# Optimization experiments

Hardware: AMD Instinct MI355X
Metric: run time of the kernel (lower is better)

The kernel has to match this reference:

```python
import jax, jax.numpy as jnp
import numpy as np

QLEN, BSZ, D_MODEL = 2048, 4, 1024
N_HEAD, D_HEAD = 16, 64
SCALE = 1.0 / D_HEAD ** 0.5


def _rope(t, cos, sin):
    # t: [len, b, n, d_head]; cos/sin: [len, d_head//2]
    tr = t.reshape(*t.shape[:-1], D_HEAD // 2, 2)
    t_r, t_i = tr[..., 0], tr[..., 1]
    c = cos[:, None, None, :]
    s = sin[:, None, None, :]
    o_r = t_r * c - t_i * s
    o_i = t_r * s + t_i * c
    return jnp.stack([o_r, o_i], axis=-1).reshape(t.shape)


def setup_inputs() -> dict:
    key = jax.random.key(0)
    ks = jax.random.split(key, 9)
    x = jax.random.normal(ks[0], (QLEN, BSZ, D_MODEL), dtype=jnp.float32)
    # standard RoPE frequencies: theta = 10000^{-2i/d_head}
    inv_freq = 1.0 / (10000.0 ** (np.arange(0, D_HEAD, 2, dtype=np.float32) / D_HEAD))
    ang = np.arange(QLEN, dtype=np.float32)[:, None] * inv_freq[None, :]
    freqs_cos = jnp.asarray(np.cos(ang))
    freqs_sin = jnp.asarray(np.sin(ang))
    init = lambda k, sh: (jax.random.normal(k, sh, dtype=jnp.float32) * 0.02)
    H = N_HEAD * D_HEAD
    return {
        "x": x,
        "freqs_cos": freqs_cos,
        "freqs_sin": freqs_sin,
        "Wq": init(ks[1], (D_MODEL, H)), "bq": jnp.zeros((H,), jnp.float32),
        "Wk": init(ks[2], (D_MODEL, H)), "bk": jnp.zeros((H,), jnp.float32),
        "Wv": init(ks[3], (D_MODEL, H)), "bv": jnp.zeros((H,), jnp.float32),
        "Wo": init(ks[4], (H, D_MODEL)), "bo": jnp.zeros((D_MODEL,), jnp.float32),
    }


def reference(x, freqs_cos, freqs_sin, Wq, bq, Wk, bk, Wv, bv, Wo, bo):
    qlen, bsz, _ = x.shape
    q = x @ Wq + bq  # [q, b, n*d]
    k = x @ Wk + bk
    v = x @ Wv + bv
    new_mem = (k, v)
    q = q.reshape(qlen, bsz, N_HEAD, D_HEAD)
    k = k.reshape(qlen, bsz, N_HEAD, D_HEAD)
    vv = v.reshape(qlen, bsz, N_HEAD, D_HEAD)
    q = _rope(q, freqs_cos, freqs_sin)
    k = _rope(k, freqs_cos, freqs_sin)
    attn = jnp.einsum('ibnd,jbnd->ijbn', q, k) * SCALE
    p = jax.nn.softmax(attn, axis=1)
    o = jnp.einsum('ijbn,jbnd->ibnd', p, vv)
    o = o.reshape(qlen, bsz, N_HEAD * D_HEAD) @ Wo + bo
    return (o, new_mem[0], new_mem[1])
```

## Files before the change

### kernel.cpp

```cpp
#include <hip/hip_runtime.h>

typedef __attribute__((ext_vector_type(2))) float f32x2;
typedef __attribute__((ext_vector_type(4))) float f32x4;
typedef __attribute__((ext_vector_type(16))) float f32x16;
typedef __attribute__((ext_vector_type(8))) __bf16 bf16x8;
typedef __attribute__((ext_vector_type(4))) __bf16 bf16x4;
typedef __attribute__((ext_vector_type(2))) __bf16 bf16x2;
typedef __attribute__((ext_vector_type(4))) unsigned int u32x4;

#define DEVI __device__ __forceinline__

static constexpr int QLEN = 2048, BSZ = 4, DM = 1024, NH = 16, DH = 64;
static constexpr int MROWS = QLEN * BSZ;
static constexpr long OSZ  = (long)MROWS * DM;
static constexpr float SCL2E = 0.125f * 1.4426950408889634f;

DEVI void gload_lds16(const void* g, void* l) {
  __builtin_amdgcn_global_load_lds(
      (__attribute__((address_space(1))) void*)(size_t)g,
      (__attribute__((address_space(3))) void*)l, 16, 0, 0);
}

DEVI f32x16 zero16() {
  f32x16 v;
#pragma unroll
  for (int i = 0; i < 16; ++i) v[i] = 0.f;
  return v;
}

DEVI unsigned pack_bf16(float lo, float hi) {
  bf16x2 v = { (__bf16)lo, (__bf16)hi };
  return __builtin_bit_cast(unsigned, v);
}

struct f2x8 { f32x2 h[8]; };

DEVI f32x2 pk_add(f32x2 a, f32x2 b) {
  f32x2 d;
  asm("v_pk_add_f32 %0, %1, %2" : "=v"(d) : "v"(a), "v"(b));
  return d;
}

__global__ void k_prep(const float* __restrict__ x, __bf16* __restrict__ xb,
                       const float* __restrict__ W0, const float* __restrict__ W1,
                       const float* __restrict__ W2, const float* __restrict__ W3,
                       __bf16* __restrict__ WtAll) {
  __shared__ float tile[64][65];
  const int t = threadIdx.x;
  if (blockIdx.x < 1024) {
    const int g = blockIdx.x >> 8;
    const float* W = g == 0 ? W0 : (g == 1 ? W1 : (g == 2 ? W2 : W3));
    __bf16* Wt = WtAll + (size_t)g * DM * DM;
    const int bid = blockIdx.x & 255;
    const int tk = bid >> 4;
    const int tn = bid & 15;
    const int r = t >> 4;
    const int c4 = (t & 15) << 2;
#pragma unroll
    for (int i = 0; i < 4; ++i) {
      const float4 v = *(const float4*)&W[(size_t)(tk * 64 + r + i * 16) * DM + tn * 64 + c4];
      tile[r + i * 16][c4 + 0] = v.x;
      tile[r + i * 16][c4 + 1] = v.y;
      tile[r + i * 16][c4 + 2] = v.z;
      tile[r + i * 16][c4 + 3] = v.w;
    }
    __syncthreads();
#pragma unroll
    for (int i = 0; i < 4; ++i) {
      const int n = r + i * 16;
      bf16x4 o = { (__bf16)tile[c4 + 0][n], (__bf16)tile[c4 + 1][n],
                   (__bf16)tile[c4 + 2][n], (__bf16)tile[c4 + 3][n] };
      *(bf16x4*)&Wt[(size_t)(tn * 64 + n) * DM + tk * 64 + c4] = o;
    }
  } else {
    const int n4 = (int)(OSZ / 4);
    int i = (blockIdx.x - 1024) * 256 + t;
    for (; i < n4; i += 2048 * 256) {
      const float4 v = ((const float4*)x)[i];
      bf16x4 o = { (__bf16)v.x, (__bf16)v.y, (__bf16)v.z, (__bf16)v.w };
      ((bf16x4*)xb)[i] = o;
    }
  }
}

__global__ __launch_bounds__(256, 4) void k_vtrans(const __bf16* __restrict__ vb,
                                                   __bf16* __restrict__ VT) {
  __shared__ __bf16 tile[128 * 72];
  const int t = threadIdx.x;
  const int bh = blockIdx.x >> 4;
  const int s0 = (blockIdx.x & 15) * 128;
  const int b = bh >> 4, h = bh & 15;

  {
    const int r = t >> 1, hh = t & 1;
    const __bf16* src = vb + (size_t)((s0 + r) * 4 + b) * DM + h * 64 + hh * 32;
    __bf16* dst = tile + r * 72 + hh * 32;
#pragma unroll
    for (int k = 0; k < 4; ++k)
      *(bf16x8*)(dst + k * 8) = *(const bf16x8*)(src + k * 8);
  }
  __syncthreads();

  const int l = t & 63;
  const int w = t >> 6;
  const int hf = l >> 5;
#pragma unroll
  for (int gi = 0; gi < 4; ++gi) {
    const int idx = w * 4 + gi;
    const int ktl = idx >> 3;
    const int fi = idx & 7;
    const int jc = fi >> 1, dh = fi & 1;
    const int d = dh * 32 + (l & 31);
    const int j8 = ktl * 64 + jc * 16 + hf * 8;
    bf16x8 pk;
#pragma unroll
    for (int jj = 0; jj < 8; ++jj) pk[jj] = tile[(j8 + jj) * 72 + d];
    const int kt_g = (blockIdx.x & 15) * 2 + ktl;
    *(bf16x8*)&VT[(size_t)(((bh * 32 + kt_g) * 8 + fi) * 64 + l) * 8] = pk;
  }
}

DEVI void gemm_tile_core(const __bf16* __restrict__ A, const __bf16* __restrict__ Bt,
                         char* Alds, char* Blds, int m0, int n0, int t,
                         f32x4 (&acc)[4][4]) {
  constexpr int K = 1024;
  const int l = t & 63;
  const int w = t >> 6;
  const int wr = w >> 1, wc = w & 1;

  int a_addr[2][4], b_addr[2][4];
#pragma unroll
  for (int s = 0; s < 2; ++s)
#pragma unroll
    for (int f = 0; f < 4; ++f) {
      const int ca = s * 64 + ((l >> 4) << 4);
      const int ra = wr * 64 + f * 16 + (l & 15);
      a_addr[s][f] = ra * 128 + (ca ^ ((ra & 7) << 4));
      const int rb = wc * 64 + f * 16 + (l & 15);
      b_addr[s][f] = rb * 128 + (ca ^ ((rb & 7) << 4));
    }

  int g_row[4], g_col[4];
#pragma unroll
  for (int i = 0; i < 4; ++i) {
    const int g = i * 256 + t;
    g_row[i] = g >> 3;
    g_col[i] = ((g & 7) ^ (g_row[i] & 7)) * 8;
  }

  for (int kt = 0; kt < K / 64; ++kt) {
#pragma unroll
    for (int i = 0; i < 4; ++i) {
      gload_lds16(A + (size_t)(m0 + g_row[i]) * K + kt * 64 + g_col[i],
                  Alds + (size_t)(i * 256 + t) * 16);
      gload_lds16(Bt + (size_t)(n0 + g_row[i]) * K + kt * 64 + g_col[i],
                  Blds + (size_t)(i * 256 + t) * 16);
    }
    __syncthreads();
#pragma unroll
    for (int s = 0; s < 2; ++s) {
      bf16x8 af[4], bfr[4];
#pragma unroll
      for (int f = 0; f < 4; ++f) {
        af[f]  = *(const bf16x8*)(Alds + a_addr[s][f]);
        bfr[f] = *(const bf16x8*)(Blds + b_addr[s][f]);
      }
      __builtin_amdgcn_s_setprio(1);
#pragma unroll
      for (int mi = 0; mi < 4; ++mi)
#pragma unroll
        for (int ni = 0; ni < 4; ++ni)
          acc[mi][ni] = __builtin_amdgcn_mfma_f32_16x16x32_bf16(af[mi], bfr[ni], acc[mi][ni], 0, 0, 0);
      __builtin_amdgcn_s_setprio(0);
    }
    __syncthreads();
  }
}

__global__ __launch_bounds__(256, 3) void k_gemm(
    const __bf16* __restrict__ A, const __bf16* __restrict__ Bt,
    const float* __restrict__ bias, float* __restrict__ Cf) {
  __shared__ alignas(16) char lds[32768];
  const int t = threadIdx.x;
  const int l = t & 63;
  const int w = t >> 6;
  const int n0 = (blockIdx.x & 7) * 128;
  const int m0 = (blockIdx.x >> 3) * 128;
  const int wr = w >> 1, wc = w & 1;

  f32x4 acc[4][4];
#pragma unroll
  for (int i = 0; i < 4; ++i)
#pragma unroll
    for (int j = 0; j < 4; ++j) acc[i][j] = (f32x4){0.f, 0.f, 0.f, 0.f};

  gemm_tile_core(A, Bt, lds, lds + 16384, m0, n0, t, acc);

  const int rowb = m0 + wr * 64 + ((l >> 4) << 2);
  const int colb = n0 + wc * 64 + (l & 15);
#pragma unroll
  for (int ni = 0; ni < 4; ++ni) {
    const float bv = bias[colb + ni * 16];
#pragma unroll
    for (int mi = 0; mi < 4; ++mi)
#pragma unroll
      for (int r = 0; r < 4; ++r)
        Cf[(size_t)(rowb + mi * 16 + r) * 1024 + colb + ni * 16] = acc[mi][ni][r] + bv;
  }
}

__global__ __launch_bounds__(256, 3) void k_gemm_qkv(
    const __bf16* __restrict__ A, const __bf16* __restrict__ Bt,
    const float* __restrict__ bq, const float* __restrict__ bk, const float* __restrict__ bv,
    const float* __restrict__ fc, const float* __restrict__ fs,
    float* __restrict__ ok, float* __restrict__ ov,
    __bf16* __restrict__ qr, __bf16* __restrict__ kr, __bf16* __restrict__ vb) {
  __shared__ alignas(16) char lds[32768];
  const int t = threadIdx.x;
  const int l = t & 63;
  const int w = t >> 6;
  const int nt = blockIdx.x % 24;
  const int n0 = nt * 128;
  const int m0 = (blockIdx.x / 24) * 128;
  const int wr = w >> 1, wc = w & 1;

  f32x4 acc[4][4];
#pragma unroll
  for (int i = 0; i < 4; ++i)
#pragma unroll
    for (int j = 0; j < 4; ++j) acc[i][j] = (f32x4){0.f, 0.f, 0.f, 0.f};

  gemm_tile_core(A, Bt, lds, lds + 16384, m0, n0, t, acc);

  const int grp = n0 >> 10;
  const int rowb = m0 + wr * 64 + ((l >> 4) << 2);
  const int colb = (n0 & 1023) + wc * 64 + (l & 15);

  if (grp == 2) {
#pragma unroll
    for (int ni = 0; ni < 4; ++ni) {
      const float bvv = bv[colb + ni * 16];
#pragma unroll
      for (int mi = 0; mi < 4; ++mi)
#pragma unroll
        for (int r = 0; r < 4; ++r) {
          const float v = acc[mi][ni][r] + bvv;
          const size_t idx = (size_t)(rowb + mi * 16 + r) * 1024 + colb + ni * 16;
          ov[idx] = v;
          vb[idx] = (__bf16)v;
        }
    }
  } else {
    const float* bias = grp == 0 ? bq : bk;
    __bf16* Rb = grp == 0 ? qr : kr;
    const float scl = grp == 0 ? SCL2E : 1.0f;
    const float sgn = (l & 1) ? 1.f : -1.f;
#pragma unroll
    for (int ni = 0; ni < 4; ++ni) {
      const int col = colb + ni * 16;
      const float bvv = bias[col];
      const int p = (col & 63) >> 1;
#pragma unroll
      for (int mi = 0; mi < 4; ++mi) {
        const int s_idx = (rowb + mi * 16) >> 2;
        const float cv = fc[s_idx * 32 + p] * scl;
        const float sv = fs[s_idx * 32 + p] * scl * sgn;
#pragma unroll
        for (int r = 0; r < 4; ++r) {
          const float v = acc[mi][ni][r] + bvv;
          if (grp == 1) ok[(size_t)(rowb + mi * 16 + r) * 1024 + col] = v;
          const float part = __shfl_xor(v, 1);
          Rb[(size_t)(rowb + mi * 16 + r) * 1024 + col] = (__bf16)(v * cv + part * sv);
        }
      }
    }
  }
}

static constexpr int FBUF11 = 16384;

__global__ __launch_bounds__(256, 4) void k_flash11(
    const __bf16* __restrict__ Q, const __bf16* __restrict__ Kr,
    const __bf16* __restrict__ VT, __bf16* __restrict__ O) {
  __shared__ alignas(16) char lds[2 * FBUF11];

  const int t = threadIdx.x, l = t & 63, w = t >> 6;
  const int hf = l >> 5;
  const int q32 = l & 31;
  const int swz = (blockIdx.x & 7) * 128 + (blockIdx.x >> 3);
  const int qt = swz & 15;
  const int bh = swz >> 4;
  const int b = bh >> 4, hd = bh & 15;

  const int qrow = qt * 128 + w * 32 + q32;

  bf16x8 qf[4];
#pragma unroll
  for (int kc = 0; kc < 4; ++kc)
    qf[kc] = *(const bf16x8*)(Q + (size_t)(qrow * 4 + b) * DM + hd * 64 + kc * 16 + hf * 8);

  const f32x16 Z = zero16();
  f32x16 acc0 = zero16(), acc1 = zero16();
  float l_run = 0.f;

  const size_t KSTRIDE = (size_t)64 * 4 * DM;
  const size_t VSTRIDE = (size_t)512 * 8;
  const __bf16* kp0 = Kr + (size_t)((t & 31) * 4 + b) * DM + hd * 64 + (t >> 5) * 8;
  const __bf16* kp1 = kp0 + (size_t)32 * 4 * DM;
  const __bf16* vp0 = VT + ((size_t)(bh * 32) * 512 + t) * 8;
  const __bf16* vp1 = vp0 + 256 * 8;

  char* const K0 = lds;
  char* const V0 = lds + 8192;
  char* const K1 = lds + FBUF11;
  char* const V1 = K1 + 8192;

#define STAGE11(Kn, Vn)                         \
  do {                                          \
    gload_lds16(kp0, (Kn) + t * 16);            \
    gload_lds16(kp1, (Kn) + 4096 + t * 16);     \
    gload_lds16(vp0, (Vn) + t * 16);            \
    gload_lds16(vp1, (Vn) + 4096 + t * 16);     \
    kp0 += KSTRIDE; kp1 += KSTRIDE;             \
    vp0 += VSTRIDE; vp1 += VSTRIDE;             \
  } while (0)

  auto PROCESS = [&](const char* Kl, const char* Vl) {
    const bf16x8 kf00 = *(const bf16x8*)(Kl + 0 * 1024 + l * 16);
    const bf16x8 kf10 = *(const bf16x8*)(Kl + 4 * 1024 + l * 16);
    __builtin_amdgcn_s_setprio(1);
    f32x16 s0 = __builtin_amdgcn_mfma_f32_32x32x16_bf16(kf00, qf[0], Z, 0, 0, 0);
    f32x16 s1 = __builtin_amdgcn_mfma_f32_32x32x16_bf16(kf10, qf[0], Z, 0, 0, 0);
#pragma unroll
    for (int kc = 1; kc < 4; ++kc) {
      const bf16x8 kf0 = *(const bf16x8*)(Kl + (0 * 4 + kc) * 1024 + l * 16);
      const bf16x8 kf1 = *(const bf16x8*)(Kl + (1 * 4 + kc) * 1024 + l * 16);
      s0 = __builtin_amdgcn_mfma_f32_32x32x16_bf16(kf0, qf[kc], s0, 0, 0, 0);
      s1 = __builtin_amdgcn_mfma_f32_32x32x16_bf16(kf1, qf[kc], s1, 0, 0, 0);
    }
    __builtin_amdgcn_s_setprio(0);

    f32x16 p0, p1;
#pragma unroll
    for (int r = 0; r < 16; ++r) {
      p0[r] = __builtin_amdgcn_exp2f(s0[r]);
      p1[r] = __builtin_amdgcn_exp2f(s1[r]);
    }

    const f2x8 P0 = __builtin_bit_cast(f2x8, p0);
    const f2x8 P1 = __builtin_bit_cast(f2x8, p1);
    f32x2 a8[8];
#pragma unroll
    for (int j = 0; j < 8; ++j) a8[j] = pk_add(P0.h[j], P1.h[j]);
#pragma unroll
    for (int j = 0; j < 4; ++j) a8[j] = pk_add(a8[j], a8[j + 4]);
    a8[0] = pk_add(a8[0], a8[2]);
    a8[1] = pk_add(a8[1], a8[3]);
    a8[0] = pk_add(a8[0], a8[1]);
    float rs = a8[0][0] + a8[0][1];
    {
      float tmp = rs;
      asm("v_permlane32_swap_b32 %0, %1" : "+v"(rs), "+v"(tmp));
      rs = rs + tmp;
    }
    l_run += rs;

    unsigned pkw[16];
#pragma unroll
    for (int j = 0; j < 8; ++j) {
      pkw[j]     = pack_bf16(P0.h[j][0], P0.h[j][1]);
      pkw[8 + j] = pack_bf16(P1.h[j][0], P1.h[j][1]);
    }

#pragma unroll
    for (int c = 0; c < 2; ++c)
#pragma unroll
      for (int jc2 = 0; jc2 < 2; ++jc2) {
        unsigned w0 = pkw[c * 8 + 4 * jc2 + 0], w2 = pkw[c * 8 + 4 * jc2 + 2];
        unsigned w1 = pkw[c * 8 + 4 * jc2 + 1], w3 = pkw[c * 8 + 4 * jc2 + 3];
        asm("v_permlane32_swap_b32 %0, %1" : "+v"(w0), "+v"(w2));
        asm("v_permlane32_swap_b32 %0, %1" : "+v"(w1), "+v"(w3));
        const u32x4 pw = { w0, w1, w2, w3 };
        const bf16x8 pf = __builtin_bit_cast(bf16x8, pw);
        const int jc = c * 2 + jc2;
        const bf16x8 vf0 = *(const bf16x8*)(Vl + (jc * 2 + 0) * 1024 + l * 16);
        const bf16x8 vf1 = *(const bf16x8*)(Vl + (jc * 2 + 1) * 1024 + l * 16);
        __builtin_amdgcn_s_setprio(1);
        acc0 = __builtin_amdgcn_mfma_f32_32x32x16_bf16(vf0, pf, acc0, 0, 0, 0);
        acc1 = __builtin_amdgcn_mfma_f32_32x32x16_bf16(vf1, pf, acc1, 0, 0, 0);
        __builtin_amdgcn_s_setprio(0);
      }
  };

  STAGE11(K0, V0);

  for (int kt = 0; kt < QLEN / 64; kt += 2) {
    __syncthreads();
    STAGE11(K1, V1);
    PROCESS(K0, V0);
    __syncthreads();
    if (kt + 2 < QLEN / 64) STAGE11(K0, V0);
    PROCESS(K1, V1);
  }
#undef STAGE11

  const float inv = 1.0f / l_run;
#pragma unroll
  for (int g = 0; g < 4; ++g) {
    {
      const int d0 = 8 * g + 4 * hf;
      bf16x4 o4 = { (__bf16)(acc0[4 * g + 0] * inv), (__bf16)(acc0[4 * g + 1] * inv),
                    (__bf16)(acc0[4 * g + 2] * inv), (__bf16)(acc0[4 * g + 3] * inv) };
      *(bf16x4*)&O[(size_t)(qrow * 4 + b) * DM + hd * 64 + d0] = o4;
    }
    {
      const int d0 = 32 + 8 * g + 4 * hf;
      bf16x4 o4 = { (__bf16)(acc1[4 * g + 0] * inv), (__bf16)(acc1[4 * g + 1] * inv),
                    (__bf16)(acc1[4 * g + 2] * inv), (__bf16)(acc1[4 * g + 3] * inv) };
      *(bf16x4*)&O[(size_t)(qrow * 4 + b) * DM + hd * 64 + d0] = o4;
    }
  }
}

extern "C" void kernel_launch(void* const* d_in, const int* in_sizes, int n_in,
                              void* d_out, int out_size, void* d_ws, size_t ws_size,
                              hipStream_t stream) {
  const float* x    = (const float*)d_in[0];
  const float* fcos = (const float*)d_in[1];
  const float* fsin = (const float*)d_in[2];
  const float* Wq   = (const float*)d_in[3];
  const float* bq   = (const float*)d_in[4];
  const float* Wk   = (const float*)d_in[5];
  const float* bk   = (const float*)d_in[6];
  const float* Wv   = (const float*)d_in[7];
  const float* bv   = (const float*)d_in[8];
  const float* Wo   = (const float*)d_in[9];
  const float* bo   = (const float*)d_in[10];

  float* out_o = (float*)d_out;
  float* out_k = out_o + OSZ;
  float* out_v = out_o + 2 * OSZ;

  char* ws = (char*)d_ws;
  __bf16* xb  = (__bf16*)(ws);
  __bf16* VT  = (__bf16*)(ws);
  __bf16* wqt = (__bf16*)(ws + 16777216);
  __bf16* wot = (__bf16*)(ws + 23068672);
  __bf16* qr  = (__bf16*)(ws + 25165824);
  __bf16* kr  = (__bf16*)(ws + 41943040);
  __bf16* vb  = (__bf16*)(ws + 58720256);
  __bf16* ao  = (__bf16*)(ws + 75497472);

  k_prep<<<3072, 256, 0, stream>>>(x, xb, Wq, Wk, Wv, Wo, wqt);

  k_gemm_qkv<<<1536, 256, 0, stream>>>(xb, wqt, bq, bk, bv, fcos, fsin,
                                       out_k, out_v, qr, kr, vb);

  k_vtrans<<<1024, 256, 0, stream>>>(vb, VT);

  k_flash11<<<1024, 256, 0, stream>>>(qr, kr, VT, ao);

  k_gemm<<<512, 256, 0, stream>>>(ao, wot, bo, out_o);
}
```

Before: 195.9 us.

## Rewrite QKV GEMM as 256x256 tile, 8-wave kernel with pipelined LDS staging

Replaces the 128x128, 4-wave QKV projection GEMM with a 256x256 tile kernel using 8 waves and 128 KB of double-buffered LDS. Global-to-LDS loads for the next k-tile are interleaved between MFMA phases, and waves raise their priority during MFMA bursts. Block indices are remapped so that neighbouring blocks share tiles, which should improve L2 reuse. The aim is higher arithmetic intensity and overlap of memory with compute, at the cost of fewer blocks (384) and heavy LDS use that limits occupancy.

New measurement: 235.0 us. +20.0%, slower.

```diff
diff --git a/kernel.cpp b/kernel.cpp
--- a/kernel.cpp
+++ b/kernel.cpp
@@ -209,39 +209,166 @@
   }
 }
 
-__global__ __launch_bounds__(256, 3) void k_gemm_qkv(
+__global__ __launch_bounds__(512, 2) void k_gemm_qkv8(
     const __bf16* __restrict__ A, const __bf16* __restrict__ Bt,
     const float* __restrict__ bq, const float* __restrict__ bk, const float* __restrict__ bv,
     const float* __restrict__ fc, const float* __restrict__ fs,
     float* __restrict__ ok, float* __restrict__ ov,
     __bf16* __restrict__ qr, __bf16* __restrict__ kr, __bf16* __restrict__ vb) {
-  __shared__ alignas(16) char lds[32768];
+  __shared__ alignas(16) char lds[131072];
   const int t = threadIdx.x;
   const int l = t & 63;
-  const int w = t >> 6;
-  const int nt = blockIdx.x % 24;
-  const int n0 = nt * 128;
-  const int m0 = (blockIdx.x / 24) * 128;
-  const int wr = w >> 1, wc = w & 1;
-
-  f32x4 acc[4][4];
-#pragma unroll
-  for (int i = 0; i < 4; ++i)
+  const int wid = t >> 6;
+  const int wr = wid >> 2;
+  const int wc = wid & 3;
+
+  const int swz = (blockIdx.x & 7) * 48 + (blockIdx.x >> 3);
+  const int mt = swz & 31;
+  const int nt = swz >> 5;
+
+  size_t aoff[2], boff[2];
+#pragma unroll
+  for (int i = 0; i < 2; ++i) {
+    const int g = i * 512 + t;
+    const int row = g >> 3;
+    const int c16 = (g & 7) ^ (row & 7);
+    aoff[i] = (size_t)(mt * 256 + row) * 1024 + c16 * 8;
+    boff[i] = (size_t)(nt * 256 + row) * 1024 + c16 * 8;
+  }
+
+  const int rowbyte = (l & 15) * 128;
+  const int ct0 = (((l >> 4) << 4)) ^ ((l & 7) << 4);
+  const int ct1 = (64 + ((l >> 4) << 4)) ^ ((l & 7) << 4);
+
+  f32x4 acc[8][4];
+#pragma unroll
+  for (int i = 0; i < 8; ++i)
 #pragma unroll
     for (int j = 0; j < 4; ++j) acc[i][j] = (f32x4){0.f, 0.f, 0.f, 0.f};
 
-  gemm_tile_core(A, Bt, lds, lds + 16384, m0, n0, t, acc);
-
-  const int grp = n0 >> 10;
-  const int rowb = m0 + wr * 64 + ((l >> 4) << 2);
-  const int colb = (n0 & 1023) + wc * 64 + (l & 15);
+  bf16x8 af[2][4], bf[2][4];
+
+  auto stageA = [&](int d, int h, int kt) {
+#pragma unroll
+    for (int i = 0; i < 2; ++i)
+      gload_lds16(A + aoff[i] + (size_t)h * 131072 + kt * 64,
+                  lds + d * 65536 + h * 16384 + (size_t)(i * 512 + t) * 16);
+  };
+  auto stageB = [&](int d, int h, int kt) {
+#pragma unroll
+    for (int i = 0; i < 2; ++i)
+      gload_lds16(Bt + boff[i] + (size_t)h * 131072 + kt * 64,
+                  lds + d * 65536 + 32768 + h * 16384 + (size_t)(i * 512 + t) * 16);
+  };
+
+  stageA(0, 0, 0); stageA(0, 1, 0);
+  stageB(0, 0, 0); stageB(0, 1, 0);
+  stageB(1, 0, 1); stageB(1, 1, 1);
+  asm volatile("s_waitcnt vmcnt(4)");
+  __builtin_amdgcn_s_barrier();
+
+  auto do_tile = [&](int T, int cur) {
+    const char* ab = lds + cur * 65536 + wr * 16384 + rowbyte;
+    const char* bb = lds + cur * 65536 + 32768 + (wc >> 1) * 16384 + (wc & 1) * 8192 + rowbyte;
+    const int nxt = cur ^ 1;
+
+#pragma unroll
+    for (int ks = 0; ks < 2; ++ks) {
+      const int ct = ks ? ct1 : ct0;
+#pragma unroll
+      for (int mm = 0; mm < 4; ++mm) af[ks][mm] = *(const bf16x8*)(ab + mm * 2048 + ct);
+#pragma unroll
+      for (int nn = 0; nn < 2; ++nn) bf[ks][nn] = *(const bf16x8*)(bb + nn * 2048 + ct);
+    }
+    if (T + 1 < 16) stageA(nxt, 0, T + 1);
+    __builtin_amdgcn_s_barrier();
+    asm volatile("s_waitcnt lgkmcnt(0)");
+    __builtin_amdgcn_sched_barrier(0);
+    __builtin_amdgcn_s_setprio(1);
+#pragma unroll
+    for (int ks = 0; ks < 2; ++ks)
+#pragma unroll
+      for (int mm = 0; mm < 4; ++mm)
+#pragma unroll
+        for (int nn = 0; nn < 2; ++nn)
+          acc[mm][nn] = __builtin_amdgcn_mfma_f32_16x16x32_bf16(af[ks][mm], bf[ks][nn], acc[mm][nn], 0, 0, 0);
+    __builtin_amdgcn_s_setprio(0);
+    __builtin_amdgcn_s_barrier();
+
+#pragma unroll
+    for (int ks = 0; ks < 2; ++ks) {
+      const int ct = ks ? ct1 : ct0;
+#pragma unroll
+      for (int nn = 2; nn < 4; ++nn) bf[ks][nn] = *(const bf16x8*)(bb + nn * 2048 + ct);
+    }
+    if (T + 1 < 16) stageA(nxt, 1, T + 1);
+    __builtin_amdgcn_s_barrier();
+    asm volatile("s_waitcnt lgkmcnt(0)");
+    __builtin_amdgcn_sched_barrier(0);
+    __builtin_amdgcn_s_setprio(1);
+#pragma unroll
+    for (int ks = 0; ks < 2; ++ks)
+#pragma unroll
+      for (int mm = 0; mm < 4; ++mm)
+#pragma unroll
+        for (int nn = 2; nn < 4; ++nn)
+          acc[mm][nn] = __builtin_amdgcn_mfma_f32_16x16x32_bf16(af[ks][mm], bf[ks][nn], acc[mm][nn], 0, 0, 0);
+    __builtin_amdgcn_s_setprio(0);
+    __builtin_amdgcn_s_barrier();
+
+#pragma unroll
+    for (int ks = 0; ks < 2; ++ks) {
+      const int ct = ks ? ct1 : ct0;
+#pragma unroll
+      for (int mm = 0; mm < 4; ++mm) af[ks][mm] = *(const bf16x8*)(ab + 8192 + mm * 2048 + ct);
+    }
+    if (T + 2 < 16) stageB(cur, 0, T + 2);
+    __builtin_amdgcn_s_barrier();
+    asm volatile("s_waitcnt lgkmcnt(0)");
+    __builtin_amdgcn_sched_barrier(0);
+    __builtin_amdgcn_s_setprio(1);
+#pragma unroll
+    for (int ks = 0; ks < 2; ++ks)
+#pragma unroll
+      for (int mm = 0; mm < 4; ++mm)
+#pragma unroll
+        for (int nn = 0; nn < 2; ++nn)
+          acc[4 + mm][nn] = __builtin_amdgcn_mfma_f32_16x16x32_bf16(af[ks][mm], bf[ks][nn], acc[4 + mm][nn], 0, 0, 0);
+    __builtin_amdgcn_s_setprio(0);
+    __builtin_amdgcn_s_barrier();
+
+    if (T + 2 < 16) stageB(cur, 1, T + 2);
+    if (T >= 14) asm volatile("s_waitcnt vmcnt(0)");
+    else         asm volatile("s_waitcnt vmcnt(4)");
+    __builtin_amdgcn_s_barrier();
+    __builtin_amdgcn_s_setprio(1);
+#pragma unroll
+    for (int ks = 0; ks < 2; ++ks)
+#pragma unroll
+      for (int mm = 0; mm < 4; ++mm)
+#pragma unroll
+        for (int nn = 2; nn < 4; ++nn)
+          acc[4 + mm][nn] = __builtin_amdgcn_mfma_f32_16x16x32_bf16(af[ks][mm], bf[ks][nn], acc[4 + mm][nn], 0, 0, 0);
+    __builtin_amdgcn_s_setprio(0);
+    __builtin_amdgcn_s_barrier();
+  };
+
+  for (int T = 0; T < 16; T += 2) {
+    do_tile(T, 0);
+    do_tile(T + 1, 1);
+  }
+
+  const int n0abs = nt * 256;
+  const int grp = n0abs >> 10;
+  const int rowb = mt * 256 + wr * 128 + ((l >> 4) << 2);
+  const int colb = (n0abs & 1023) + wc * 64 + (l & 15);
 
   if (grp == 2) {
 #pragma unroll
     for (int ni = 0; ni < 4; ++ni) {
       const float bvv = bv[colb + ni * 16];
 #pragma unroll
-      for (int mi = 0; mi < 4; ++mi)
+      for (int mi = 0; mi < 8; ++mi)
 #pragma unroll
         for (int r = 0; r < 4; ++r) {
           const float v = acc[mi][ni][r] + bvv;
@@ -261,7 +388,7 @@
       const float bvv = bias[col];
       const int p = (col & 63) >> 1;
 #pragma unroll
-      for (int mi = 0; mi < 4; ++mi) {
+      for (int mi = 0; mi < 8; ++mi) {
         const int s_idx = (rowb + mi * 16) >> 2;
         const float cv = fc[s_idx * 32 + p] * scl;
         const float sv = fs[s_idx * 32 + p] * scl * sgn;
@@ -453,7 +580,7 @@
 
   k_prep<<<3072, 256, 0, stream>>>(x, xb, Wq, Wk, Wv, Wo, wqt);
 
-  k_gemm_qkv<<<1536, 256, 0, stream>>>(xb, wqt, bq, bk, bv, fcos, fsin,
+  k_gemm_qkv8<<<384, 512, 0, stream>>>(xb, wqt, bq, bk, bv, fcos, fsin,
                                        out_k, out_v, qr, kr, vb);
 
   k_vtrans<<<1024, 256, 0, stream>>>(vb, VT);
```
